# Kernel optimization log

Hardware: AMD Instinct MI355X
Metric: run time of the kernel (lower is better)

Reference implementation:

```python
import jax, jax.numpy as jnp
import numpy as np

B, T = 64, 512
N = B * T            # 32768 influencer nodes (one per timestep)
E = 524288           # edges, avg in-degree 16
D_IN, H1, H2 = 256, 128, 128
D = H1 + H2          # GRU input dim (concat of conv1/conv2 outputs)
RH = 256             # GRU hidden


def setup_inputs() -> dict:
    key = jax.random.key(0)
    ks = jax.random.split(key, 20)
    def gp(k, shape, fan):
        return jax.random.normal(k, shape, jnp.float32) / np.float32(np.sqrt(fan))
    return {
        "x": jax.random.normal(ks[0], (N, D_IN), jnp.float32),
        "edge_index": jax.random.randint(ks[1], (2, E), 0, N, jnp.int32),
        "lengths": jnp.maximum(jax.random.randint(ks[2], (B,), 0, T, jnp.int32), 1),
        # GATConv layer 1 (bipartite lin_src/lin_dst, heads=1)
        "Wsrc1": gp(ks[3], (D_IN, H1), D_IN), "Wdst1": gp(ks[4], (D_IN, H1), D_IN),
        "asrc1": gp(ks[5], (H1,), H1), "adst1": gp(ks[6], (H1,), H1),
        "b1": jnp.zeros((H1,), jnp.float32),
        # GATConv layer 2
        "Wsrc2": gp(ks[7], (H1, H2), H1), "Wdst2": gp(ks[8], (H1, H2), H1),
        "asrc2": gp(ks[9], (H2,), H2), "adst2": gp(ks[10], (H2,), H2),
        "b2": jnp.zeros((H2,), jnp.float32),
        # GRU (PyTorch gate order r,z,n)
        "Wi": gp(ks[11], (D, 3 * RH), D), "Wh": gp(ks[12], (RH, 3 * RH), RH),
        "bi": jnp.zeros((3 * RH,), jnp.float32), "bh": jnp.zeros((3 * RH,), jnp.float32),
        # attention + MLP head
        "w_att": gp(ks[13], (RH,), RH), "b_att": jnp.zeros((), jnp.float32),
        "fc1_w": gp(ks[14], (RH, RH // 2), RH), "fc1_b": jnp.zeros((RH // 2,), jnp.float32),
        "fc2_w": gp(ks[15], (RH // 2, 1), RH // 2), "fc2_b": jnp.zeros((1,), jnp.float32),
    }


def _gat(x, src, dst, Wsrc, Wdst, a_src, a_dst, b):
    # GATConv, heads=1, no self loops: softmax of leaky_relu attention over in-edges.
    hs = x @ Wsrc                                   # [N,H] source messages
    hd = x @ Wdst                                   # [N,H] dest features
    al = (hs @ a_src)[src] + (hd @ a_dst)[dst]      # [E]
    al = jax.nn.leaky_relu(al, 0.2)
    m = jax.ops.segment_max(al, dst, num_segments=N)
    ex = jnp.exp(al - m[dst])
    den = jax.ops.segment_sum(ex, dst, num_segments=N)
    w = ex / (den[dst] + 1e-16)
    out = jax.ops.segment_sum(w[:, None] * hs[src], dst, num_segments=N)
    return out + b


def reference(x, edge_index, lengths, Wsrc1, Wdst1, asrc1, adst1, b1,
              Wsrc2, Wdst2, asrc2, adst2, b2, Wi, Wh, bi, bh,
              w_att, b_att, fc1_w, fc1_b, fc2_w, fc2_b):
    src, dst = edge_index[0], edge_index[1]
    # HeteroGNN: conv1 -> relu -> (dropout=eval identity) -> conv2 -> concat
    h1 = jax.nn.relu(_gat(x, src, dst, Wsrc1, Wdst1, asrc1, adst1, b1))
    h2 = _gat(h1, src, dst, Wsrc2, Wdst2, asrc2, adst2, b2)
    emb = jnp.concatenate([h1, h2], axis=1).reshape(B, T, D)
    # GRU over T steps (batch_first); packed padding irrelevant: attention masks pads
    xg = emb @ Wi + bi                               # [B,T,3RH] precomputed input gates
    def step(h, xg_t):
        gh = h @ Wh + bh
        xr, xz, xn = jnp.split(xg_t, 3, axis=-1)
        hr, hz, hn = jnp.split(gh, 3, axis=-1)
        r = jax.nn.sigmoid(xr + hr)
        z = jax.nn.sigmoid(xz + hz)
        n = jnp.tanh(xn + r * hn)
        h = (1.0 - z) * n + z * h
        return h, h
    h0 = jnp.zeros((B, RH), emb.dtype)
    _, hseq = jax.lax.scan(step, h0, jnp.swapaxes(xg, 0, 1))
    hseq = jnp.swapaxes(hseq, 0, 1)                  # [B,T,RH]
    # SimpleAttention: masked softmax pooling over time
    scores = hseq @ w_att + b_att                    # [B,T]
    mask = jnp.arange(T)[None, :] < lengths[:, None]
    scores = jnp.where(mask, scores, -1e9)
    wts = jax.nn.softmax(scores, axis=1)
    ctx = jnp.einsum('bt,bth->bh', wts, hseq)        # [B,RH]
    z1 = jax.nn.relu(ctx @ fc1_w + fc1_b)
    return (z1 @ fc2_w + fc2_b).squeeze(-1)          # [B]
```

## Files before the change

kernel.cpp:

```cpp
#include <hip/hip_runtime.h>
#include <hip/hip_bf16.h>
#include <hip/hip_fp16.h>
#include <math.h>

#define N_NODES 32768
#define N_EDGES 524288
#define BATCH 64
#define SEQT 512

typedef _Float16 h2_t __attribute__((ext_vector_type(2)));

__device__ __forceinline__ float wave_reduce_sum(float v){
  #pragma unroll
  for (int o = 32; o > 0; o >>= 1) v += __shfl_down(v, o, 64);
  return v;
}

__device__ __forceinline__ unsigned pack2_f16(float lo, float hi){
  unsigned l = (unsigned)__half_as_ushort(__float2half_rn(lo));
  unsigned h = (unsigned)__half_as_ushort(__float2half_rn(hi));
  return l | (h << 16);
}

__device__ __forceinline__ float fdot2(unsigned w, unsigned h, float acc){
  return __builtin_amdgcn_fdot2(__builtin_bit_cast(h2_t, w),
                                __builtin_bit_cast(h2_t, h), acc, false);
}

__global__ void k_vdst(const float* __restrict__ Wdst1, const float* __restrict__ adst1,
                       const float* __restrict__ Wdst2, const float* __restrict__ adst2,
                       float* __restrict__ vdst){
  int t = threadIdx.x;
  if (t < 256){
    float s = 0.f;
    for (int j = 0; j < 128; j++) s += Wdst1[t*128+j]*adst1[j];
    vdst[t] = s;
  }
  if (t < 128){
    float s = 0.f;
    for (int j = 0; j < 128; j++) s += Wdst2[t*128+j]*adst2[j];
    vdst[256+t] = s;
  }
}

__global__ void k_gemm128(const float* __restrict__ X, int ldx, int Kd,
                          const float* __restrict__ W, float* __restrict__ hs){
  __shared__ float Xs[16*256];
  int n0 = blockIdx.x * 16;
  int tid = threadIdx.x;
  for (int r = 0; r < 16; r++)
    for (int k = tid; k < Kd; k += 256)
      Xs[r*Kd + k] = X[(long)(n0+r)*ldx + k];
  __syncthreads();
  int c = tid & 127, rg = tid >> 7;
  float acc[8] = {0,0,0,0,0,0,0,0};
  for (int k = 0; k < Kd; k++){
    float wv = W[k*128 + c];
    #pragma unroll
    for (int r = 0; r < 8; r++) acc[r] += Xs[(rg*8+r)*Kd + k] * wv;
  }
  #pragma unroll
  for (int r = 0; r < 8; r++) hs[(long)(n0 + rg*8 + r)*128 + c] = acc[r];
}

__global__ void k_sd(const float* __restrict__ hs, const float* __restrict__ asrc,
                     const float* __restrict__ X, int ldx, int Kd, const float* __restrict__ vd,
                     float* __restrict__ sv, float* __restrict__ dv){
  int n = blockIdx.x*4 + (threadIdx.x >> 6);
  int l = threadIdx.x & 63;
  float p = hs[(long)n*128 + l]*asrc[l] + hs[(long)n*128 + 64 + l]*asrc[64+l];
  float q = X[(long)n*ldx + l]*vd[l] + X[(long)n*ldx + 64 + l]*vd[64+l];
  if (Kd == 256)
    q += X[(long)n*ldx + 128 + l]*vd[128+l] + X[(long)n*ldx + 192 + l]*vd[192+l];
  p = wave_reduce_sum(p);
  q = wave_reduce_sum(q);
  if (l == 0){ sv[n] = p; dv[n] = q; }
}

__global__ void k_hist(const int* __restrict__ dst, int* __restrict__ cnt){
  int e = blockIdx.x*256 + threadIdx.x;
  if (e < N_EDGES) atomicAdd(&cnt[dst[e]], 1);
}

__global__ void k_scan(int* __restrict__ cnt, int* __restrict__ off){
  __shared__ int part[1024];
  int t = threadIdx.x;
  int base_i = t*32;
  int s = 0;
  #pragma unroll
  for (int i = 0; i < 32; i++) s += cnt[base_i + i];
  part[t] = s;
  __syncthreads();
  for (int o = 1; o < 1024; o <<= 1){
    int v = (t >= o) ? part[t-o] : 0;
    __syncthreads();
    part[t] += v;
    __syncthreads();
  }
  int run = part[t] - s;
  for (int i = 0; i < 32; i++){
    off[base_i + i] = run;
    run += cnt[base_i + i];
    cnt[base_i + i] = 0;
  }
  if (t == 1023) off[N_NODES] = part[1023];
}

__global__ void k_scatter(const int* __restrict__ dst, const int* __restrict__ off,
                          int* __restrict__ cnt, int* __restrict__ eid){
  int e = blockIdx.x*256 + threadIdx.x;
  if (e < N_EDGES){
    int d0 = dst[e];
    int pos = off[d0] + atomicAdd(&cnt[d0], 1);
    eid[pos] = e;
  }
}

__global__ void k_agg(const int* __restrict__ eid, const int* __restrict__ off,
                      const int* __restrict__ src,
                      const float* __restrict__ sv, const float* __restrict__ dv,
                      const float* __restrict__ hs, const float* __restrict__ bias,
                      float* __restrict__ emb, int colOff, int doRelu){
  int n = blockIdx.x*4 + (threadIdx.x >> 6);
  int l = threadIdx.x & 63;
  int eb = off[n], ee = off[n+1];
  float dn = dv[n];
  float m = -1e30f, den = 0.f, a0 = 0.f, a1 = 0.f;
  for (int i = eb; i < ee; i++){
    int e = eid[i];
    int sn = src[e];
    float al = sv[sn] + dn;
    al = al > 0.f ? al : 0.2f*al;
    float nm = fmaxf(m, al);
    float scl = __expf(m - nm);
    float p   = __expf(al - nm);
    den = den*scl + p;
    a0  = a0*scl + p*hs[(long)sn*128 + l];
    a1  = a1*scl + p*hs[(long)sn*128 + 64 + l];
    m = nm;
  }
  float inv = 1.f/(den + 1e-16f);
  float v0 = a0*inv + bias[l];
  float v1 = a1*inv + bias[64+l];
  if (doRelu){ v0 = fmaxf(v0, 0.f); v1 = fmaxf(v1, 0.f); }
  emb[(long)n*256 + colOff + l] = v0;
  emb[(long)n*256 + colOff + 64 + l] = v1;
}

__global__ void k_xg(const float* __restrict__ emb, const float* __restrict__ Wi,
                     const float* __restrict__ bi, float* __restrict__ xg){
  __shared__ float Xs[16*256];
  int n0 = blockIdx.x*16;
  int tid = threadIdx.x;
  for (int r = 0; r < 16; r++)
    for (int k = tid; k < 256; k += 256)
      Xs[r*256 + k] = emb[(long)(n0+r)*256 + k];
  __syncthreads();
  float acc[16][3];
  #pragma unroll
  for (int r = 0; r < 16; r++){ acc[r][0]=0.f; acc[r][1]=0.f; acc[r][2]=0.f; }
  for (int k = 0; k < 256; k++){
    float w0 = Wi[k*768 + tid];
    float w1 = Wi[k*768 + 256 + tid];
    float w2 = Wi[k*768 + 512 + tid];
    #pragma unroll
    for (int r = 0; r < 16; r++){
      float xv = Xs[r*256 + k];
      acc[r][0] += xv*w0; acc[r][1] += xv*w1; acc[r][2] += xv*w2;
    }
  }
  float bv0 = bi[tid], bv1 = bi[256+tid], bv2 = bi[512+tid];
  #pragma unroll
  for (int r = 0; r < 16; r++){
    long rowp = (long)(n0+r)*768;
    xg[rowp + tid]       = acc[r][0] + bv0;
    xg[rowp + 256 + tid] = acc[r][1] + bv1;
    xg[rowp + 512 + tid] = acc[r][2] + bv2;
  }
}

__attribute__((amdgpu_waves_per_eu(2, 2)))
__global__ void __launch_bounds__(512, 2)
k_gru4(const float* __restrict__ xg,
       const float* __restrict__ Wh, const float* __restrict__ bh,
       float* __restrict__ hseq){
  __shared__ __align__(16) unsigned hp_hi[128];
  __shared__ __align__(16) unsigned hp_lo[128];
  __shared__ float pr[256], pz[256], pn[256];

  int t = threadIdx.x;
  int j = t & 255;
  int half = t >> 8;
  int b = blockIdx.x;

  unsigned wr[64], wz[64], wn[64];
  {
    const float* W0 = Wh + (long)(half*128)*768;
    #pragma unroll
    for (int m = 0; m < 64; m++){
      wr[m] = pack2_f16(W0[(2*m)*768 + j],       W0[(2*m+1)*768 + j]);
      wz[m] = pack2_f16(W0[(2*m)*768 + 256 + j], W0[(2*m+1)*768 + 256 + j]);
      wn[m] = pack2_f16(W0[(2*m)*768 + 512 + j], W0[(2*m+1)*768 + 512 + j]);
    }
  }

  if (t < 128){ hp_hi[t] = 0u; hp_lo[t] = 0u; }
  float bhr = 0.f, bhz = 0.f, bhn = 0.f;
  if (half == 0){ bhr = bh[j]; bhz = bh[256 + j]; bhn = bh[512 + j]; }
  float hreg = 0.f;
  __syncthreads();

  const uint4* hi4 = ((const uint4*)hp_hi) + half*16;
  const uint4* lo4 = ((const uint4*)hp_lo) + half*16;

  for (int t_step = 0; t_step < SEQT; t_step++){
    float xr = 0.f, xz = 0.f, xn = 0.f;
    if (half == 0){
      long rowp = ((long)b*SEQT + t_step)*768;
      xr = xg[rowp + j];
      xz = xg[rowp + 256 + j];
      xn = xg[rowp + 512 + j];
    }

    float ar0 = 0.f, ar1 = 0.f, az0 = 0.f, az1 = 0.f, an0 = 0.f, an1 = 0.f;
    #pragma unroll
    for (int q = 0; q < 16; q++){
      uint4 hh = hi4[q];
      uint4 hl = lo4[q];
      ar0 = fdot2(wr[4*q+0], hh.x, ar0);
      ar1 = fdot2(wr[4*q+1], hh.y, ar1);
      ar0 = fdot2(wr[4*q+2], hh.z, ar0);
      ar1 = fdot2(wr[4*q+3], hh.w, ar1);
      az0 = fdot2(wz[4*q+0], hh.x, az0);
      az1 = fdot2(wz[4*q+1], hh.y, az1);
      az0 = fdot2(wz[4*q+2], hh.z, az0);
      az1 = fdot2(wz[4*q+3], hh.w, az1);
      an0 = fdot2(wn[4*q+0], hh.x, an0);
      an1 = fdot2(wn[4*q+1], hh.y, an1);
      an0 = fdot2(wn[4*q+2], hh.z, an0);
      an1 = fdot2(wn[4*q+3], hh.w, an1);
      ar0 = fdot2(wr[4*q+0], hl.x, ar0);
      ar1 = fdot2(wr[4*q+1], hl.y, ar1);
      ar0 = fdot2(wr[4*q+2], hl.z, ar0);
      ar1 = fdot2(wr[4*q+3], hl.w, ar1);
      az0 = fdot2(wz[4*q+0], hl.x, az0);
      az1 = fdot2(wz[4*q+1], hl.y, az1);
      az0 = fdot2(wz[4*q+2], hl.z, az0);
      az1 = fdot2(wz[4*q+3], hl.w, az1);
      an0 = fdot2(wn[4*q+0], hl.x, an0);
      an1 = fdot2(wn[4*q+1], hl.y, an1);
      an0 = fdot2(wn[4*q+2], hl.z, an0);
      an1 = fdot2(wn[4*q+3], hl.w, an1);
    }
    float ar = ar0 + ar1, az = az0 + az1, an = an0 + an1;

    if (half == 1){ pr[j] = ar; pz[j] = az; pn[j] = an; }
    __syncthreads();

    if (half == 0){
      float ghr = ar + pr[j] + bhr;
      float ghz = az + pz[j] + bhz;
      float ghn = an + pn[j] + bhn;
      float r = 1.f/(1.f + __expf(-(xr + ghr)));
      float z = 1.f/(1.f + __expf(-(xz + ghz)));
      float nn = tanhf(xn + r*ghn);
      float hv = (1.f - z)*nn + z*hreg;
      hreg = hv;
      hseq[((long)b*SEQT + t_step)*256 + j] = hv;

      float partner = __shfl_xor(hv, 1, 64);
      if ((j & 1) == 0){
        float res  = hv      - __half2float(__float2half_rn(hv));
        float resp = partner - __half2float(__float2half_rn(partner));
        hp_hi[j >> 1] = pack2_f16(hv, partner);
        hp_lo[j >> 1] = pack2_f16(res, resp);
      }
    }
    __syncthreads();
  }
}

__global__ void k_scores(const float* __restrict__ hseq, const float* __restrict__ w_att,
                         const float* __restrict__ b_att, float* __restrict__ scores){
  int n = blockIdx.x*4 + (threadIdx.x >> 6);
  int l = threadIdx.x & 63;
  const float* hp = hseq + (long)n*256;
  float p = hp[l]*w_att[l] + hp[64+l]*w_att[64+l]
          + hp[128+l]*w_att[128+l] + hp[192+l]*w_att[192+l];
  p = wave_reduce_sum(p);
  if (l == 0) scores[n] = p + b_att[0];
}

__global__ void k_final(const float* __restrict__ scores, const int* __restrict__ lengths,
                        const float* __restrict__ hseq,
                        const float* __restrict__ fc1_w, const float* __restrict__ fc1_b,
                        const float* __restrict__ fc2_w, const float* __restrict__ fc2_b,
                        float* __restrict__ out){
  __shared__ float sc[512];
  __shared__ float red[256];
  __shared__ float ctxs[256];
  __shared__ float z1s[128];
  int b = blockIdx.x, t = threadIdx.x;
  int len = lengths[b];
  for (int i = t; i < 512; i += 256){
    float v = scores[b*512 + i];
    sc[i] = (i < len) ? v : -1e9f;
  }
  __syncthreads();
  red[t] = fmaxf(sc[t], sc[t+256]);
  __syncthreads();
  for (int o = 128; o > 0; o >>= 1){
    if (t < o) red[t] = fmaxf(red[t], red[t+o]);
    __syncthreads();
  }
  float m = red[0];
  __syncthreads();
  float e0 = __expf(sc[t] - m), e1 = __expf(sc[t+256] - m);
  red[t] = e0 + e1;
  __syncthreads();
  for (int o = 128; o > 0; o >>= 1){
    if (t < o) red[t] += red[t+o];
    __syncthreads();
  }
  float den = red[0];
  __syncthreads();
  sc[t] = e0/den; sc[t+256] = e1/den;
  __syncthreads();
  float acc = 0.f;
  for (int i = 0; i < 512; i++) acc += sc[i]*hseq[((long)b*512 + i)*256 + t];
  ctxs[t] = acc;
  __syncthreads();
  if (t < 128){
    float a = fc1_b[t];
    for (int k = 0; k < 256; k++) a += ctxs[k]*fc1_w[k*128 + t];
    z1s[t] = fmaxf(a, 0.f);
  }
  __syncthreads();
  if (t < 64){
    float p = z1s[t]*fc2_w[t] + z1s[t+64]*fc2_w[t+64];
    p = wave_reduce_sum(p);
    if (t == 0) out[b] = p + fc2_b[0];
  }
}

extern "C" void kernel_launch(void* const* d_in, const int* in_sizes, int n_in,
                              void* d_out, int out_size, void* d_ws, size_t ws_size,
                              hipStream_t stream) {
  const float* x     = (const float*)d_in[0];
  const int*   edge  = (const int*)d_in[1];
  const int*   lengths = (const int*)d_in[2];
  const float* Wsrc1 = (const float*)d_in[3];
  const float* Wdst1 = (const float*)d_in[4];
  const float* asrc1 = (const float*)d_in[5];
  const float* adst1 = (const float*)d_in[6];
  const float* b1    = (const float*)d_in[7];
  const float* Wsrc2 = (const float*)d_in[8];
  const float* Wdst2 = (const float*)d_in[9];
  const float* asrc2 = (const float*)d_in[10];
  const float* adst2 = (const float*)d_in[11];
  const float* b2    = (const float*)d_in[12];
  const float* Wi    = (const float*)d_in[13];
  const float* Wh    = (const float*)d_in[14];
  const float* bi    = (const float*)d_in[15];
  const float* bh    = (const float*)d_in[16];
  const float* w_att = (const float*)d_in[17];
  const float* b_att = (const float*)d_in[18];
  const float* fc1_w = (const float*)d_in[19];
  const float* fc1_b = (const float*)d_in[20];
  const float* fc2_w = (const float*)d_in[21];
  const float* fc2_b = (const float*)d_in[22];
  float* out = (float*)d_out;

  const int* srcp = edge;
  const int* dstp = edge + N_EDGES;

  float* ws   = (float*)d_ws;
  float* emb  = ws;
  float* xg   = emb  + (size_t)N_NODES*256;
  float* hseq = xg   + (size_t)N_NODES*768;
  float* hs   = hseq + (size_t)N_NODES*256;
  float* sv   = hs   + (size_t)N_NODES*128;
  float* dv   = sv   + N_NODES;
  float* vdst = dv   + N_NODES;
  float* scores = vdst + 384;
  int* csr_cnt = (int*)(scores + N_NODES);
  int* csr_off = csr_cnt + N_NODES;
  int* csr_eid = csr_off + N_NODES + 1;

  hipMemsetAsync(csr_cnt, 0, N_NODES*sizeof(int), stream);
  k_vdst<<<1, 256, 0, stream>>>(Wdst1, adst1, Wdst2, adst2, vdst);

  k_gemm128<<<N_NODES/16, 256, 0, stream>>>(x, 256, 256, Wsrc1, hs);
  k_sd<<<N_NODES/4, 256, 0, stream>>>(hs, asrc1, x, 256, 256, vdst, sv, dv);
  k_hist<<<N_EDGES/256, 256, 0, stream>>>(dstp, csr_cnt);
  k_scan<<<1, 1024, 0, stream>>>(csr_cnt, csr_off);
  k_scatter<<<N_EDGES/256, 256, 0, stream>>>(dstp, csr_off, csr_cnt, csr_eid);
  k_agg<<<N_NODES/4, 256, 0, stream>>>(csr_eid, csr_off, srcp, sv, dv, hs, b1, emb, 0, 1);

  k_gemm128<<<N_NODES/16, 256, 0, stream>>>(emb, 256, 128, Wsrc2, hs);
  k_sd<<<N_NODES/4, 256, 0, stream>>>(hs, asrc2, emb, 256, 128, vdst+256, sv, dv);
  k_agg<<<N_NODES/4, 256, 0, stream>>>(csr_eid, csr_off, srcp, sv, dv, hs, b2, emb, 128, 0);

  k_xg<<<N_NODES/16, 256, 0, stream>>>(emb, Wi, bi, xg);
  k_gru4<<<BATCH, 512, 0, stream>>>(xg, Wh, bh, hseq);

  k_scores<<<N_NODES/4, 256, 0, stream>>>(hseq, w_att, b_att, scores);
  k_final<<<BATCH, 256, 0, stream>>>(scores, lengths, hseq, fc1_w, fc1_b, fc2_w, fc2_b, out);
}
```

Measured before the change: 1.649 ms.

## Split GRU recurrent matvec across four thread groups per batch block

The GRU recurrence kernel now uses 1024 threads per block instead of 512. The hidden dimension is split into four quarters of 64 rows, so each thread holds half as many packed fp16 weight registers and does half the dot-product work per step. Three of the quarters write partial sums to shared memory and the first quarter reduces them and applies the gate math. This shortens the serial per-step chain on the 64 blocks, at the cost of more shared-memory traffic and a wider barrier, and it may push up register pressure at the larger block size.

Result: slower. 1.726 ms (+4.7%).

```diff
diff --git a/kernel.cpp b/kernel.cpp
--- a/kernel.cpp
+++ b/kernel.cpp
@@ -179,25 +179,24 @@
   }
 }
 
-__attribute__((amdgpu_waves_per_eu(2, 2)))
-__global__ void __launch_bounds__(512, 2)
-k_gru4(const float* __restrict__ xg,
+__global__ void __launch_bounds__(1024)
+k_gru5(const float* __restrict__ xg,
        const float* __restrict__ Wh, const float* __restrict__ bh,
        float* __restrict__ hseq){
   __shared__ __align__(16) unsigned hp_hi[128];
   __shared__ __align__(16) unsigned hp_lo[128];
-  __shared__ float pr[256], pz[256], pn[256];
+  __shared__ float part[3][3][256];
 
   int t = threadIdx.x;
   int j = t & 255;
-  int half = t >> 8;
+  int q4 = t >> 8;
   int b = blockIdx.x;
 
-  unsigned wr[64], wz[64], wn[64];
+  unsigned wr[32], wz[32], wn[32];
   {
-    const float* W0 = Wh + (long)(half*128)*768;
+    const float* W0 = Wh + (long)(q4*64)*768;
     #pragma unroll
-    for (int m = 0; m < 64; m++){
+    for (int m = 0; m < 32; m++){
       wr[m] = pack2_f16(W0[(2*m)*768 + j],       W0[(2*m+1)*768 + j]);
       wz[m] = pack2_f16(W0[(2*m)*768 + 256 + j], W0[(2*m+1)*768 + 256 + j]);
       wn[m] = pack2_f16(W0[(2*m)*768 + 512 + j], W0[(2*m+1)*768 + 512 + j]);
@@ -206,17 +205,17 @@
 
   if (t < 128){ hp_hi[t] = 0u; hp_lo[t] = 0u; }
   float bhr = 0.f, bhz = 0.f, bhn = 0.f;
-  if (half == 0){ bhr = bh[j]; bhz = bh[256 + j]; bhn = bh[512 + j]; }
+  if (q4 == 0){ bhr = bh[j]; bhz = bh[256 + j]; bhn = bh[512 + j]; }
   float hreg = 0.f;
   __syncthreads();
 
-  const uint4* hi4 = ((const uint4*)hp_hi) + half*16;
-  const uint4* lo4 = ((const uint4*)hp_lo) + half*16;
-
-  for (int t_step = 0; t_step < SEQT; t_step++){
+  const uint4* hi4 = ((const uint4*)hp_hi) + q4*8;
+  const uint4* lo4 = ((const uint4*)hp_lo) + q4*8;
+
+  for (int ts = 0; ts < SEQT; ts++){
     float xr = 0.f, xz = 0.f, xn = 0.f;
-    if (half == 0){
-      long rowp = ((long)b*SEQT + t_step)*768;
+    if (q4 == 0){
+      long rowp = ((long)b*SEQT + ts)*768;
       xr = xg[rowp + j];
       xz = xg[rowp + 256 + j];
       xn = xg[rowp + 512 + j];
@@ -224,7 +223,7 @@
 
     float ar0 = 0.f, ar1 = 0.f, az0 = 0.f, az1 = 0.f, an0 = 0.f, an1 = 0.f;
     #pragma unroll
-    for (int q = 0; q < 16; q++){
+    for (int q = 0; q < 8; q++){
       uint4 hh = hi4[q];
       uint4 hl = lo4[q];
       ar0 = fdot2(wr[4*q+0], hh.x, ar0);
@@ -254,19 +253,19 @@
     }
     float ar = ar0 + ar1, az = az0 + az1, an = an0 + an1;
 
-    if (half == 1){ pr[j] = ar; pz[j] = az; pn[j] = an; }
-    __syncthreads();
-
-    if (half == 0){
-      float ghr = ar + pr[j] + bhr;
-      float ghz = az + pz[j] + bhz;
-      float ghn = an + pn[j] + bhn;
+    if (q4){ part[q4-1][0][j] = ar; part[q4-1][1][j] = az; part[q4-1][2][j] = an; }
+    __syncthreads();
+
+    if (q4 == 0){
+      float ghr = ar + part[0][0][j] + part[1][0][j] + part[2][0][j] + bhr;
+      float ghz = az + part[0][1][j] + part[1][1][j] + part[2][1][j] + bhz;
+      float ghn = an + part[0][2][j] + part[1][2][j] + part[2][2][j] + bhn;
       float r = 1.f/(1.f + __expf(-(xr + ghr)));
       float z = 1.f/(1.f + __expf(-(xz + ghz)));
       float nn = tanhf(xn + r*ghn);
       float hv = (1.f - z)*nn + z*hreg;
       hreg = hv;
-      hseq[((long)b*SEQT + t_step)*256 + j] = hv;
+      hseq[((long)b*SEQT + ts)*256 + j] = hv;
 
       float partner = __shfl_xor(hv, 1, 64);
       if ((j & 1) == 0){
@@ -402,7 +401,7 @@
   k_agg<<<N_NODES/4, 256, 0, stream>>>(csr_eid, csr_off, srcp, sv, dv, hs, b2, emb, 128, 0);
 
   k_xg<<<N_NODES/16, 256, 0, stream>>>(emb, Wi, bi, xg);
-  k_gru4<<<BATCH, 512, 0, stream>>>(xg, Wh, bh, hseq);
+  k_gru5<<<BATCH, 1024, 0, stream>>>(xg, Wh, bh, hseq);
 
   k_scores<<<N_NODES/4, 256, 0, stream>>>(hseq, w_att, b_att, scores);
   k_final<<<BATCH, 256, 0, stream>>>(scores, lengths, hseq, fc1_w, fc1_b, fc2_w, fc2_b, out);
```
